# Performance work log

Hardware: AMD Instinct MI355X
Metric: run time of the kernel (lower is better)

Reference implementation:

```python
import jax, jax.numpy as jnp
import numpy as np

L, H, NH, HD, FF, S, B, V, NL = 2, 2048, 16, 128, 4096, 1024, 2, 32000, 4
R, SCALING, BLK = 2, 16.0 / 2.0, 64  # LoRA r=2, alpha=16 -> scaling 8; NF4 blocksize 64
NF4 = jnp.array([-1.0, -0.6961928009986877, -0.5250730514526367, -0.39491748809814453,
                 -0.28444138169288635, -0.18477343022823334, -0.09105003625154495, 0.0,
                 0.07958029955625534, 0.16093020141124725, 0.24611230194568634,
                 0.33791524171829224, 0.44070982933044434, 0.5626170039176941,
                 0.7229568362236023, 1.0], dtype=jnp.float32)

def dequant(codes, scales):
    # codes [out, in] int -> NF4 values; scales [out, in//BLK] absmax per 64-block
    return NF4[codes] * jnp.repeat(scales, BLK, axis=-1)

def qlin(x, codes, scales, A, Bm):
    # fused dequant + GEMM + LoRA low-rank update: x @ (Wd + s*B@A).T
    W = dequant(codes, scales)
    return x @ W.T + SCALING * ((x @ A.T) @ Bm.T)

def layer_norm(x, g, b):
    mu = jnp.mean(x, -1, keepdims=True)
    var = jnp.var(x, -1, keepdims=True)
    return (x - mu) * jax.lax.rsqrt(var + 1e-5) * g + b

def rope(x):  # x [B,S,NH,HD]
    half = HD // 2
    inv = 1.0 / (10000.0 ** (jnp.arange(half, dtype=jnp.float32) / half))
    ang = jnp.arange(S, dtype=jnp.float32)[:, None] * inv[None, :]
    cos = jnp.concatenate([jnp.cos(ang)] * 2, -1)[None, :, None, :]
    sin = jnp.concatenate([jnp.sin(ang)] * 2, -1)[None, :, None, :]
    x1, x2 = x[..., :half], x[..., half:]
    return x * cos + jnp.concatenate([-x2, x1], -1) * sin

def setup_inputs() -> dict:
    key = jax.random.key(0)
    it = iter(jax.random.split(key, 64))
    nrm = lambda shp, s: jax.random.normal(next(it), shp, jnp.float32) * s
    cod = lambda shp: jax.random.randint(next(it), shp, 0, 16, jnp.int32)
    scl = lambda shp: jax.random.uniform(next(it), shp, jnp.float32) * 0.02 + 1e-3
    lens = jax.random.randint(next(it), (B,), S // 2, S + 1)
    return dict(
        input_ids=jax.random.randint(next(it), (B, S), 0, V, jnp.int32),
        attention_mask=(jnp.arange(S)[None, :] < lens[:, None]).astype(jnp.int32),
        labels=jax.random.randint(next(it), (B,), 0, NL, jnp.int32),
        embed=nrm((V, H), 0.02),
        qkv_codes=cod((L, 3 * H, H)), qkv_scales=scl((L, 3 * H, H // BLK)),
        qkv_A=nrm((L, R, H), 0.01), qkv_B=nrm((L, 3 * H, R), 0.01),
        dense_codes=cod((L, H, H)), dense_scales=scl((L, H, H // BLK)),
        dense_A=nrm((L, R, H), 0.01), dense_B=nrm((L, H, R), 0.01),
        min_codes=cod((L, 2 * FF, H)), min_scales=scl((L, 2 * FF, H // BLK)),
        min_A=nrm((L, R, H), 0.01), min_B=nrm((L, 2 * FF, R), 0.01),
        mout_codes=cod((L, H, FF)), mout_scales=scl((L, H, FF // BLK)),
        mout_A=nrm((L, R, FF), 0.01), mout_B=nrm((L, H, R), 0.01),
        ln1_g=jnp.ones((L, H)), ln1_b=jnp.zeros((L, H)),
        ln2_g=jnp.ones((L, H)), ln2_b=jnp.zeros((L, H)),
        lnf_g=jnp.ones((H,)), lnf_b=jnp.zeros((H,)),
        classifier_w=nrm((NL, H), 0.01),
    )

def reference(input_ids, attention_mask, labels, embed, qkv_codes, qkv_scales, qkv_A, qkv_B,
              dense_codes, dense_scales, dense_A, dense_B, min_codes, min_scales, min_A, min_B,
              mout_codes, mout_scales, mout_A, mout_B, ln1_g, ln1_b, ln2_g, ln2_b,
              lnf_g, lnf_b, classifier_w):
    x = embed[input_ids]  # [B,S,H]
    mask = jnp.tril(jnp.ones((S, S), bool))[None, None] & (attention_mask[:, None, None, :] > 0)
    for l in range(L):
        h = layer_norm(x, ln1_g[l], ln1_b[l])
        qkv = qlin(h, qkv_codes[l], qkv_scales[l], qkv_A[l], qkv_B[l]).reshape(B, S, NH, 3 * HD)
        q, k, v = qkv[..., :HD], qkv[..., HD:2 * HD], qkv[..., 2 * HD:]
        q, k = rope(q), rope(k)
        scores = jnp.einsum('bqhd,bkhd->bhqk', q, k) / np.float32(np.sqrt(HD))
        probs = jax.nn.softmax(jnp.where(mask, scores, jnp.float32(-1e30)), -1)
        attn = jnp.einsum('bhqk,bkhd->bqhd', probs, v).reshape(B, S, H)
        x = x + qlin(attn, dense_codes[l], dense_scales[l], dense_A[l], dense_B[l])
        h2 = layer_norm(x, ln2_g[l], ln2_b[l])
        u = qlin(h2, min_codes[l], min_scales[l], min_A[l], min_B[l])  # [B,S,2*FF] packed SwiGLU
        g = jax.nn.silu(u[..., :FF]) * u[..., FF:]
        x = x + qlin(g, mout_codes[l], mout_scales[l], mout_A[l], mout_B[l])
    x = layer_norm(x, lnf_g, lnf_b)
    eos = x[jnp.arange(B), attention_mask.sum(1) - 1]  # last non-padded token hidden
    logits = eos @ classifier_w.T
    logp = jax.nn.log_softmax(logits, -1)
    loss = -jnp.mean(logp[jnp.arange(B), labels])
    return loss, logits
```

## Files before the change

kernel.cpp:

```cpp
#include <hip/hip_runtime.h>

typedef unsigned short u16;
typedef __attribute__((ext_vector_type(4))) float f32x4;
typedef __attribute__((ext_vector_type(8))) short short8;
typedef __attribute__((ext_vector_type(4))) short short4v;

constexpr int CL  = 2;
constexpr int CH  = 2048;
constexpr int CNH = 16;
constexpr int CHD = 128;
constexpr int CFF = 4096;
constexpr int CS  = 1024;
constexpr int CB  = 2;
constexpr int CNL = 4;
constexpr int CM  = CB * CS;
#define SCALING 8.0f

__device__ __constant__ float NF4TAB[16] = {
    -1.0f, -0.6961928009986877f, -0.5250730514526367f, -0.39491748809814453f,
    -0.28444138169288635f, -0.18477343022823334f, -0.09105003625154495f, 0.0f,
    0.07958029955625534f, 0.16093020141124725f, 0.24611230194568634f,
    0.33791524171829224f, 0.44070982933044434f, 0.5626170039176941f,
    0.7229568362236023f, 1.0f};

__device__ __forceinline__ u16 f2bf(float f) {
  union { float f; unsigned u; } v; v.f = f;
  unsigned r = v.u + 0x7fffu + ((v.u >> 16) & 1u);
  return (u16)(r >> 16);
}
__device__ __forceinline__ float bf2f(u16 u) {
  union { unsigned u; float f; } v; v.u = ((unsigned)u) << 16;
  return v.f;
}

template <int N> __device__ __forceinline__ void wait_vm() {
  if constexpr (N == 0)      asm volatile("s_waitcnt vmcnt(0)" ::: "memory");
  else if constexpr (N == 6) asm volatile("s_waitcnt vmcnt(6)" ::: "memory");
  else if constexpr (N == 8) asm volatile("s_waitcnt vmcnt(8)" ::: "memory");
  else                       asm volatile("s_waitcnt vmcnt(0)" ::: "memory");
}

__device__ __forceinline__ float blockReduceSum(float v) {
  __shared__ float sh[4];
  #pragma unroll
  for (int o = 32; o > 0; o >>= 1) v += __shfl_down(v, o);
  __syncthreads();
  if ((threadIdx.x & 63) == 0) sh[threadIdx.x >> 6] = v;
  __syncthreads();
  return sh[0] + sh[1] + sh[2] + sh[3];
}

__global__ void k_embed(const int* __restrict__ ids, const float* __restrict__ emb,
                        float* __restrict__ x) {
  int m = blockIdx.x;
  const float4* src = (const float4*)(emb + (size_t)ids[m] * CH);
  float4* dst = (float4*)(x + (size_t)m * CH);
  for (int i = threadIdx.x; i < CH / 4; i += 256) dst[i] = src[i];
}

__global__ void k_ln_xa(const float* __restrict__ x, const float* __restrict__ g,
                        const float* __restrict__ b, const float* __restrict__ A,
                        u16* __restrict__ o, float* __restrict__ xA) {
  int m = blockIdx.x, tid = threadIdx.x;
  const float* row = x + (size_t)m * CH;
  float s = 0.f, s2 = 0.f;
  for (int i = tid; i < CH / 4; i += 256) {
    float4 v = ((const float4*)row)[i];
    s += v.x + v.y + v.z + v.w;
    s2 += v.x * v.x + v.y * v.y + v.z * v.z + v.w * v.w;
  }
  s = blockReduceSum(s);
  s2 = blockReduceSum(s2);
  float mu = s / CH, var = s2 / CH - mu * mu;
  float rs = rsqrtf(var + 1e-5f);
  u16* orow = o + (size_t)m * CH;
  float s0 = 0.f, s1 = 0.f;
  for (int i = tid; i < CH / 4; i += 256) {
    float4 v = ((const float4*)row)[i];
    float4 gv = ((const float4*)g)[i];
    float4 bv = ((const float4*)b)[i];
    float4 a0 = ((const float4*)A)[i];
    float4 a1 = ((const float4*)(A + CH))[i];
    float h0 = (v.x - mu) * rs * gv.x + bv.x;
    float h1 = (v.y - mu) * rs * gv.y + bv.y;
    float h2 = (v.z - mu) * rs * gv.z + bv.z;
    float h3 = (v.w - mu) * rs * gv.w + bv.w;
    short4v ov = { (short)f2bf(h0), (short)f2bf(h1), (short)f2bf(h2), (short)f2bf(h3) };
    *(short4v*)(orow + i * 4) = ov;
    s0 += h0 * a0.x + h1 * a0.y + h2 * a0.z + h3 * a0.w;
    s1 += h0 * a1.x + h1 * a1.y + h2 * a1.z + h3 * a1.w;
  }
  s0 = blockReduceSum(s0);
  s1 = blockReduceSum(s1);
  if (tid == 0) { xA[2 * m] = s0; xA[2 * m + 1] = s1; }
}

__global__ void k_xa(const u16* __restrict__ xb, const float* __restrict__ A,
                     float* __restrict__ xA, int K) {
  int m = blockIdx.x, tid = threadIdx.x;
  const u16* row = xb + (size_t)m * K;
  float s0 = 0.f, s1 = 0.f;
  for (int c = tid; c < K / 8; c += 256) {
    short8 v = *(const short8*)(row + c * 8);
    #pragma unroll
    for (int e = 0; e < 8; ++e) {
      float f = bf2f((u16)v[e]);
      s0 += f * A[c * 8 + e];
      s1 += f * A[K + c * 8 + e];
    }
  }
  s0 = blockReduceSum(s0);
  s1 = blockReduceSum(s1);
  if (tid == 0) { xA[2 * m] = s0; xA[2 * m + 1] = s1; }
}

__global__ void k_dequant(const int* __restrict__ codes, const float* __restrict__ scales,
                          u16* __restrict__ w, int kshift, long total) {
  __shared__ float lut[16];
  if (threadIdx.x < 16) lut[threadIdx.x] = NF4TAB[threadIdx.x];
  __syncthreads();
  long base = ((long)blockIdx.x * 256 + threadIdx.x) * 8;
  if (base >= total) return;
  long n = base >> kshift;
  int k = (int)(base & ((1L << kshift) - 1));
  float sc = scales[(size_t)n * (1 << (kshift - 6)) + (k >> 6)];
  const int* cp = codes + base;
  short8 o;
  #pragma unroll
  for (int i = 0; i < 8; ++i) o[i] = (short)f2bf(lut[cp[i] & 15] * sc);
  *(short8*)(w + base) = o;
}

__global__ void k_ropetab(float* __restrict__ cosT, float* __restrict__ sinT) {
  int i = blockIdx.x * 256 + threadIdx.x;
  if (i >= CS * 64) return;
  int s = i >> 6, d = i & 63;
  float inv = powf(10000.0f, -(float)d / 64.0f);
  float a = (float)s * inv;
  cosT[i] = cosf(a);
  sinT[i] = sinf(a);
}

__global__ void k_rope(const u16* __restrict__ qkv, const float* __restrict__ cosT,
                       const float* __restrict__ sinT, u16* __restrict__ Qb,
                       u16* __restrict__ Kb) {
  int bid = blockIdx.x;
  int s = bid & (CS - 1);
  int z = bid >> 10;
  int b = z >> 4, h = z & 15;
  int d = threadIdx.x;
  const u16* base = qkv + ((size_t)(b * CS + s)) * (3 * CH) + h * (3 * CHD);
  int dh = d & 63;
  float c = cosT[s * 64 + dh], sn = sinT[s * 64 + dh];
  float sgn = (d < 64) ? -1.0f : 1.0f;
  float q = bf2f(base[d]),       qp = bf2f(base[d ^ 64]);
  float k = bf2f(base[CHD + d]), kp = bf2f(base[CHD + (d ^ 64)]);
  size_t oi = ((size_t)z * CS + s) * CHD + d;
  Qb[oi] = f2bf(q * c + sgn * qp * sn);
  Kb[oi] = f2bf(k * c + sgn * kp * sn);
}

__global__ void k_vtrans(const u16* __restrict__ qkv, u16* __restrict__ Vt) {
  __shared__ u16 tile[32][33];
  int z = blockIdx.z;
  int b = z >> 4, h = z & 15;
  int s0 = blockIdx.x * 32, d0 = blockIdx.y * 32;
  int tx = threadIdx.x, ty = threadIdx.y;
  #pragma unroll
  for (int i = 0; i < 32; i += 8)
    tile[ty + i][tx] =
        qkv[((size_t)(b * CS + s0 + ty + i)) * (3 * CH) + h * (3 * CHD) + 2 * CHD + d0 + tx];
  __syncthreads();
  #pragma unroll
  for (int i = 0; i < 32; i += 8)
    Vt[((size_t)z * CHD + d0 + ty + i) * CS + s0 + tx] = tile[tx][ty + i];
}

__global__ __launch_bounds__(256, 2) void k_flash(
    const u16* __restrict__ Qb, const u16* __restrict__ Kb, const u16* __restrict__ Vt,
    const int* __restrict__ amask, u16* __restrict__ out) {
  __shared__ u16 Ks[64 * 128];
  __shared__ u16 Vs[128 * 64];
  __shared__ float bias[CS];
  __shared__ u16 Ps[4][16][80];
  int bid = blockIdx.x;
  int qt = 15 - (bid >> 5);
  int z = bid & 31;
  int b = z >> 4, h = z & 15;
  int tid = threadIdx.x, lane = tid & 63, wid = tid >> 6;
  int lrow = lane & 15, lgrp = lane >> 4;
  const u16* Qz = Qb + (size_t)z * CS * CHD;
  const u16* Kz = Kb + (size_t)z * CS * CHD;
  const u16* Vz = Vt + (size_t)z * CHD * CS;

  for (int i = tid; i < CS; i += 256)
    bias[i] = amask[b * CS + i] ? 0.f : -1e30f;

  int qrow = qt * 64 + wid * 16 + lrow;
  short8 qf[4];
  #pragma unroll
  for (int kk = 0; kk < 4; ++kk)
    qf[kk] = *(const short8*)(Qz + (size_t)qrow * CHD + kk * 32 + lgrp * 8);

  float m_r[4], l_r[4];
  #pragma unroll
  for (int r = 0; r < 4; ++r) { m_r[r] = -3e38f; l_r[r] = 0.f; }
  f32x4 o_acc[8];
  #pragma unroll
  for (int dj = 0; dj < 8; ++dj) o_acc[dj] = (f32x4){0.f, 0.f, 0.f, 0.f};

  const float SCL = 0.08838834764831845f;

  short8 kA[4], vA[4];
  #pragma unroll
  for (int it = 0; it < 4; ++it) {
    int c = it * 256 + tid;
    kA[it] = *(const short8*)(Kz + (size_t)(c >> 4) * CHD + (c & 15) * 8);
    vA[it] = *(const short8*)(Vz + (size_t)(c >> 3) * CS + (c & 7) * 8);
  }

  for (int t = 0; t <= qt; ++t) {
    int k0 = t * 64;
    __syncthreads();
    #pragma unroll
    for (int it = 0; it < 4; ++it) {
      int c = it * 256 + tid;
      int key = c >> 4, ch = c & 15;
      *(short8*)((char*)Ks + key * 256 + ((ch * 16) ^ ((key & 7) << 4))) = kA[it];
      int d = c >> 3, ch2 = c & 7;
      *(short8*)((char*)Vs + d * 128 + ((ch2 * 16) ^ ((d & 7) << 4))) = vA[it];
    }
    short8 kB[4], vB[4];
    if (t < qt) {
      int k1 = k0 + 64;
      #pragma unroll
      for (int it = 0; it < 4; ++it) {
        int c = it * 256 + tid;
        kB[it] = *(const short8*)(Kz + (size_t)(k1 + (c >> 4)) * CHD + (c & 15) * 8);
        vB[it] = *(const short8*)(Vz + (size_t)(c >> 3) * CS + k1 + (c & 7) * 8);
      }
    }
    __syncthreads();

    f32x4 s_acc[4];
    #pragma unroll
    for (int nj = 0; nj < 4; ++nj) s_acc[nj] = (f32x4){0.f, 0.f, 0.f, 0.f};
    #pragma unroll
    for (int kk = 0; kk < 4; ++kk) {
      #pragma unroll
      for (int nj = 0; nj < 4; ++nj) {
        int key = nj * 16 + lrow;
        short8 kf = *(const short8*)((const char*)Ks + key * 256 +
                                     (((kk * 32 + lgrp * 8) * 2) ^ ((key & 7) << 4)));
        s_acc[nj] = __builtin_amdgcn_mfma_f32_16x16x32_bf16(qf[kk], kf, s_acc[nj], 0, 0, 0);
      }
    }

    bool diag = (t == qt);
    float p[4][4], mx[4];
    #pragma unroll
    for (int r = 0; r < 4; ++r) {
      int ql = wid * 16 + 4 * lgrp + r;
      float rm = -3e38f;
      #pragma unroll
      for (int nj = 0; nj < 4; ++nj) {
        int kl = nj * 16 + lrow;
        float v = s_acc[nj][r] * SCL + bias[k0 + kl];
        if (diag && kl > ql) v = -1e30f;
        p[nj][r] = v;
        rm = fmaxf(rm, v);
      }
      mx[r] = rm;
    }
    #pragma unroll
    for (int o = 1; o < 16; o <<= 1)
      #pragma unroll
      for (int r = 0; r < 4; ++r) mx[r] = fmaxf(mx[r], __shfl_xor(mx[r], o));
    float ps[4], alpha[4];
    #pragma unroll
    for (int r = 0; r < 4; ++r) {
      float mn = fmaxf(m_r[r], mx[r]);
      alpha[r] = __expf(m_r[r] - mn);
      m_r[r] = mn;
      float acc = 0.f;
      #pragma unroll
      for (int nj = 0; nj < 4; ++nj) {
        float e = __expf(p[nj][r] - mn);
        p[nj][r] = e;
        acc += e;
      }
      ps[r] = acc;
    }
    #pragma unroll
    for (int o = 1; o < 16; o <<= 1)
      #pragma unroll
      for (int r = 0; r < 4; ++r) ps[r] += __shfl_xor(ps[r], o);
    #pragma unroll
    for (int r = 0; r < 4; ++r) {
      l_r[r] = l_r[r] * alpha[r] + ps[r];
      #pragma unroll
      for (int dj = 0; dj < 8; ++dj) o_acc[dj][r] *= alpha[r];
    }

    #pragma unroll
    for (int r = 0; r < 4; ++r)
      #pragma unroll
      for (int nj = 0; nj < 4; ++nj)
        Ps[wid][4 * lgrp + r][nj * 16 + lrow] = f2bf(p[nj][r]);
    #pragma unroll
    for (int kk2 = 0; kk2 < 2; ++kk2) {
      short8 pa = *(const short8*)(&Ps[wid][lrow][kk2 * 32 + lgrp * 8]);
      #pragma unroll
      for (int dj = 0; dj < 8; ++dj) {
        int d = dj * 16 + lrow;
        short8 vf = *(const short8*)((const char*)Vs + d * 128 +
                                     (((kk2 * 32 + lgrp * 8) * 2) ^ ((d & 7) << 4)));
        o_acc[dj] = __builtin_amdgcn_mfma_f32_16x16x32_bf16(pa, vf, o_acc[dj], 0, 0, 0);
      }
    }

    if (t < qt) {
      #pragma unroll
      for (int it = 0; it < 4; ++it) { kA[it] = kB[it]; vA[it] = vB[it]; }
    }
  }

  #pragma unroll
  for (int r = 0; r < 4; ++r) {
    float inv = 1.0f / l_r[r];
    int qg = qt * 64 + wid * 16 + 4 * lgrp + r;
    size_t rowoff = ((size_t)(b * CS + qg)) * CH + h * CHD;
    #pragma unroll
    for (int dj = 0; dj < 8; ++dj)
      out[rowoff + dj * 16 + lrow] = f2bf(o_acc[dj][r] * inv);
  }
}

__global__ void k_silu_xa(const u16* __restrict__ u, const float* __restrict__ A,
                          u16* __restrict__ g, float* __restrict__ xA) {
  int m = blockIdx.x, tid = threadIdx.x;
  const u16* urow = u + (size_t)m * (2 * CFF);
  u16* grow = g + (size_t)m * CFF;
  float s0 = 0.f, s1 = 0.f;
  for (int c = tid; c < CFF / 8; c += 256) {
    short8 va = *(const short8*)(urow + c * 8);
    short8 vb = *(const short8*)(urow + CFF + c * 8);
    short8 og;
    #pragma unroll
    for (int e = 0; e < 8; ++e) {
      float a = bf2f((u16)va[e]);
      float bb = bf2f((u16)vb[e]);
      float gg = (a / (1.0f + __expf(-a))) * bb;
      og[e] = (short)f2bf(gg);
      s0 += gg * A[c * 8 + e];
      s1 += gg * A[CFF + c * 8 + e];
    }
    *(short8*)(grow + c * 8) = og;
  }
  s0 = blockReduceSum(s0);
  s1 = blockReduceSum(s1);
  if (tid == 0) { xA[2 * m] = s0; xA[2 * m + 1] = s1; }
}

template <int BM, int BN, int TW, int WM, int WN, int OUT_BF16, int LORA, int RESID>
__global__ __launch_bounds__(TW, 2) void k_gemm3(
    const u16* __restrict__ Ag, const u16* __restrict__ Bg, void* __restrict__ Cout,
    const float* __restrict__ resid, const float* __restrict__ xA,
    const float* __restrict__ lB, int K, int N) {
  constexpr int WROWS = BM / WM, WCOLS = BN / WN;
  constexpr int M_REP = WROWS / 16, N_REP = WCOLS / 16;
  constexpr int LA = BM * 8 / TW, LBN = BN * 8 / TW;
  constexpr int LPT = LA + LBN;
  __shared__ __align__(16) u16 As[2][BM * 64];
  __shared__ __align__(16) u16 Bs[2][BN * 64];
  int tid = threadIdx.x, lane = tid & 63, wid = tid >> 6;
  int wm = wid / WN, wn = wid % WN;
  int gx = gridDim.x, nwg = gx * gridDim.y;
  int bid = blockIdx.y * gx + blockIdx.x;
  int qq = nwg >> 3, rr = nwg & 7;
  int xcd = bid & 7, lid = bid >> 3;
  int swz = (xcd < rr ? xcd * (qq + 1) : rr * (qq + 1) + (xcd - rr) * qq) + lid;
  long bm = (long)(swz % gx) * BM, bn = (long)(swz / gx) * BN;

  f32x4 acc[M_REP][N_REP];
  #pragma unroll
  for (int i = 0; i < M_REP; ++i)
    #pragma unroll
    for (int j = 0; j < N_REP; ++j) acc[i][j] = (f32x4){0.f, 0.f, 0.f, 0.f};

  auto stage = [&](int buf, int t) {
    int k0 = t * 64;
    #pragma unroll
    for (int i = 0; i < LA; ++i) {
      int f = i * TW + tid;
      int r = f >> 3, g = (f & 7) ^ (r & 7);
      __builtin_amdgcn_global_load_lds(
          (const __attribute__((address_space(1))) void*)(Ag + (size_t)(bm + r) * K + k0 + g * 8),
          (__attribute__((address_space(3))) void*)(&As[buf][f * 8]), 16, 0, 0);
    }
    #pragma unroll
    for (int i = 0; i < LBN; ++i) {
      int f = i * TW + tid;
      int r = f >> 3, g = (f & 7) ^ (r & 7);
      __builtin_amdgcn_global_load_lds(
          (const __attribute__((address_space(1))) void*)(Bg + (size_t)(bn + r) * K + k0 + g * 8),
          (__attribute__((address_space(3))) void*)(&Bs[buf][f * 8]), 16, 0, 0);
    }
  };

  int NT = K >> 6;
  stage(0, 0);
  stage(1, 1);

  int kg = lane >> 4, lr = lane & 15;
  for (int t = 0; t < NT; ++t) {
    int buf = t & 1;
    if (t + 1 < NT) wait_vm<LPT>();
    else            wait_vm<0>();
    __builtin_amdgcn_s_barrier();

    short8 af[2][M_REP], bfr[2][N_REP];
    #pragma unroll
    for (int kk = 0; kk < 2; ++kk) {
      int au = kk * 4 + kg;
      #pragma unroll
      for (int i = 0; i < M_REP; ++i) {
        int r = wm * WROWS + i * 16 + lr;
        af[kk][i] = *(const short8*)(&As[buf][r * 64 + ((au ^ (r & 7)) << 3)]);
      }
      #pragma unroll
      for (int j = 0; j < N_REP; ++j) {
        int r = wn * WCOLS + j * 16 + lr;
        bfr[kk][j] = *(const short8*)(&Bs[buf][r * 64 + ((au ^ (r & 7)) << 3)]);
      }
    }
    asm volatile("s_waitcnt lgkmcnt(0)" ::: "memory");
    __builtin_amdgcn_s_barrier();
    if (t + 2 < NT) stage(buf, t + 2);

    __builtin_amdgcn_s_setprio(1);
    #pragma unroll
    for (int kk = 0; kk < 2; ++kk)
      #pragma unroll
      for (int i = 0; i < M_REP; ++i)
        #pragma unroll
        for (int j = 0; j < N_REP; ++j)
          acc[i][j] = __builtin_amdgcn_mfma_f32_16x16x32_bf16(af[kk][i], bfr[kk][j], acc[i][j], 0, 0, 0);
    __builtin_amdgcn_s_setprio(0);
  }

  #pragma unroll
  for (int i = 0; i < M_REP; ++i) {
    #pragma unroll
    for (int r = 0; r < 4; ++r) {
      long m = bm + wm * WROWS + i * 16 + ((lane >> 4) << 2) + r;
      float xa0 = 0.f, xa1 = 0.f;
      if (LORA) { xa0 = xA[2 * m]; xa1 = xA[2 * m + 1]; }
      #pragma unroll
      for (int j = 0; j < N_REP; ++j) {
        long n = bn + wn * WCOLS + j * 16 + (lane & 15);
        float v = acc[i][j][r];
        if (LORA) v += SCALING * (xa0 * lB[2 * n] + xa1 * lB[2 * n + 1]);
        if (RESID) v += resid[m * N + n];
        if (OUT_BF16)
          ((u16*)Cout)[m * N + n] = f2bf(v);
        else
          ((float*)Cout)[m * N + n] = v;
      }
    }
  }
}

#define RD_A(d, mh)                                                              \
  { _Pragma("unroll") for (int kk = 0; kk < 2; ++kk) {                           \
      _Pragma("unroll") for (int ii = 0; ii < 4; ++ii) {                         \
        int ra = ((mh) * 4 + ii) * 16 + lr;                                      \
        int slot = (kk * 4 + kg) ^ (ra & 7);                                     \
        a_f[kk][ii] = *(const short8*)(&As[d][wm][ra * 64 + slot * 8]);          \
      } } }
#define RD_B(d, nh)                                                              \
  { _Pragma("unroll") for (int kk = 0; kk < 2; ++kk) {                           \
      _Pragma("unroll") for (int jj = 0; jj < 2; ++jj) {                         \
        int rb = (wn & 1) * 64 + ((nh) * 2 + jj) * 16 + lr;                      \
        int slot = (kk * 4 + kg) ^ (rb & 7);                                     \
        b_f[nh][kk][jj] = *(const short8*)(&Bs[d][wn >> 1][rb * 64 + slot * 8]); \
      } } }
#define MFMA_Q(mh, nh)                                                           \
  { __builtin_amdgcn_s_setprio(1);                                               \
    _Pragma("unroll") for (int kk = 0; kk < 2; ++kk) {                           \
      _Pragma("unroll") for (int ii = 0; ii < 4; ++ii) {                         \
        _Pragma("unroll") for (int jj = 0; jj < 2; ++jj) {                       \
          acc[(mh) * 4 + ii][(nh) * 2 + jj] =                                    \
              __builtin_amdgcn_mfma_f32_16x16x32_bf16(                           \
                  a_f[kk][ii], b_f[nh][kk][jj],                                  \
                  acc[(mh) * 4 + ii][(nh) * 2 + jj], 0, 0, 0);                   \
        } } }                                                                    \
    __builtin_amdgcn_s_setprio(0); }
#define LGKM0_SB                                                                 \
  asm volatile("s_waitcnt lgkmcnt(0)" ::: "memory");                             \
  __builtin_amdgcn_sched_barrier(0);
#define BAR __builtin_amdgcn_s_barrier();

__global__ __launch_bounds__(512, 2) void k_gemm8(
    const u16* __restrict__ Ag, const u16* __restrict__ Bg, u16* __restrict__ Cout,
    const float* __restrict__ xA, const float* __restrict__ lB, int K, int N) {
  __shared__ __align__(16) u16 As[2][2][128 * 64];
  __shared__ __align__(16) u16 Bs[2][2][128 * 64];
  int tid = threadIdx.x, lane = tid & 63, wid = tid >> 6;
  int wm = wid >> 2, wn = wid & 3;
  int kg = lane >> 4, lr = lane & 15;
  int gx = gridDim.x, nwg = gx * gridDim.y;
  int bid = blockIdx.y * gx + blockIdx.x;
  int qq = nwg >> 3, rr = nwg & 7;
  int xcd = bid & 7, lid = bid >> 3;
  int swz = (xcd < rr ? xcd * (qq + 1) : rr * (qq + 1) + (xcd - rr) * qq) + lid;
  long bm = (long)(swz % gx) * 256, bn = (long)(swz / gx) * 256;
  const int NKT = K >> 6;

  f32x4 acc[8][4];
  #pragma unroll
  for (int i = 0; i < 8; ++i)
    #pragma unroll
    for (int j = 0; j < 4; ++j) acc[i][j] = (f32x4){0.f, 0.f, 0.f, 0.f};
  short8 a_f[2][4], b_f[2][2][2];

  auto stA = [&](int t, int h) {
    int d = t & 1;
    int tt = t < NKT ? t : NKT - 1;
    int k0 = tt << 6;
    #pragma unroll
    for (int ld = 0; ld < 2; ++ld) {
      int f = ld * 512 + tid;
      int row = f >> 3, p = f & 7;
      int ss = p ^ (row & 7);
      __builtin_amdgcn_global_load_lds(
          (const __attribute__((address_space(1))) void*)(Ag + (size_t)(bm + h * 128 + row) * K + k0 + ss * 8),
          (__attribute__((address_space(3))) void*)(&As[d][h][f * 8]), 16, 0, 0);
    }
  };
  auto stB = [&](int t, int h) {
    int d = t & 1;
    int tt = t < NKT ? t : NKT - 1;
    int k0 = tt << 6;
    #pragma unroll
    for (int ld = 0; ld < 2; ++ld) {
      int f = ld * 512 + tid;
      int row = f >> 3, p = f & 7;
      int ss = p ^ (row & 7);
      __builtin_amdgcn_global_load_lds(
          (const __attribute__((address_space(1))) void*)(Bg + (size_t)(bn + h * 128 + row) * K + k0 + ss * 8),
          (__attribute__((address_space(3))) void*)(&Bs[d][h][f * 8]), 16, 0, 0);
    }
  };

  stA(0, 0); stA(0, 1); stB(0, 0); stB(0, 1);
  stB(1, 0); stA(1, 0);
  asm volatile("s_waitcnt vmcnt(4)" ::: "memory");
  BAR

  int NI = NKT >> 1;
  for (int j = 0; j < NI; ++j) {
    int t0 = 2 * j;
    RD_A(0, 0) RD_B(0, 0)
    stA(t0 + 1, 1);
    BAR LGKM0_SB MFMA_Q(0, 0) BAR
    RD_B(0, 1)
    stB(t0 + 1, 1);
    BAR LGKM0_SB MFMA_Q(0, 1) BAR
    RD_A(0, 1)
    stB(t0 + 2, 0);
    BAR LGKM0_SB MFMA_Q(1, 0) BAR
    stA(t0 + 2, 0);
    asm volatile("s_waitcnt vmcnt(4)" ::: "memory");
    BAR MFMA_Q(1, 1) BAR
    RD_A(1, 0) RD_B(1, 0)
    stA(t0 + 2, 1);
    BAR LGKM0_SB MFMA_Q(0, 0) BAR
    RD_B(1, 1)
    stB(t0 + 2, 1);
    BAR LGKM0_SB MFMA_Q(0, 1) BAR
    RD_A(1, 1)
    stB(t0 + 3, 0);
    BAR LGKM0_SB MFMA_Q(1, 0) BAR
    stA(t0 + 3, 0);
    asm volatile("s_waitcnt vmcnt(4)" ::: "memory");
    BAR MFMA_Q(1, 1) BAR
  }

  #pragma unroll
  for (int i = 0; i < 8; ++i) {
    #pragma unroll
    for (int r = 0; r < 4; ++r) {
      long m = bm + wm * 128 + i * 16 + ((lane >> 4) << 2) + r;
      float xa0 = xA[2 * m], xa1 = xA[2 * m + 1];
      #pragma unroll
      for (int j = 0; j < 4; ++j) {
        long n = bn + wn * 64 + j * 16 + (lane & 15);
        float v = acc[i][j][r] + SCALING * (xa0 * lB[2 * n] + xa1 * lB[2 * n + 1]);
        Cout[m * N + n] = f2bf(v);
      }
    }
  }
}

__global__ void k_final(const float* __restrict__ x, const int* __restrict__ amask,
                        const int* __restrict__ labels, const float* __restrict__ g,
                        const float* __restrict__ bb, const float* __restrict__ cw,
                        float* __restrict__ out) {
  __shared__ float xr[CH];
  __shared__ float lg[CB][CNL];
  int tid = threadIdx.x;
  for (int b = 0; b < CB; ++b) {
    float fc = 0.f;
    for (int k = tid; k < CS; k += 256) fc += (amask[b * CS + k] != 0) ? 1.0f : 0.0f;
    int len = (int)(blockReduceSum(fc) + 0.5f);
    const float* row = x + ((size_t)b * CS + (len - 1)) * CH;
    float s = 0.f, s2 = 0.f;
    for (int k = tid; k < CH; k += 256) { float v = row[k]; s += v; s2 += v * v; }
    s = blockReduceSum(s);
    s2 = blockReduceSum(s2);
    float mu = s / CH, var = s2 / CH - mu * mu;
    float rs = rsqrtf(var + 1e-5f);
    for (int k = tid; k < CH; k += 256) xr[k] = (row[k] - mu) * rs * g[k] + bb[k];
    __syncthreads();
    for (int c = 0; c < CNL; ++c) {
      float p = 0.f;
      for (int k = tid; k < CH; k += 256) p += xr[k] * cw[c * CH + k];
      p = blockReduceSum(p);
      if (tid == 0) { lg[b][c] = p; out[1 + b * CNL + c] = p; }
    }
    __syncthreads();
  }
  if (tid == 0) {
    float loss = 0.f;
    for (int b = 0; b < CB; ++b) {
      float mx = -1e30f;
      for (int c = 0; c < CNL; ++c) mx = fmaxf(mx, lg[b][c]);
      float se = 0.f;
      for (int c = 0; c < CNL; ++c) se += expf(lg[b][c] - mx);
      float lse = mx + logf(se);
      loss -= (lg[b][labels[b]] - lse);
    }
    out[0] = loss / CB;
  }
}

static constexpr size_t X_OFF  = 0;
static constexpr size_t H_OFF  = X_OFF + (size_t)CM * CH * 4;
static constexpr size_t W_OFF  = H_OFF + (size_t)CM * CH * 2;
static constexpr size_t SC_OFF = W_OFF + (size_t)8192 * 2048 * 2;
static constexpr size_t PR_OFF = SC_OFF + (size_t)32 * CS * CS * 4;
static constexpr size_t XA_OFF = PR_OFF + (size_t)32 * CS * CS * 2;
static constexpr size_t CS_OFF = XA_OFF + (size_t)CM * 2 * 4;
static constexpr size_t SN_OFF = CS_OFF + (size_t)CS * 64 * 4;
static constexpr size_t WS_END = SN_OFF + (size_t)CS * 64 * 4;

extern "C" void kernel_launch(void* const* d_in, const int* in_sizes, int n_in,
                              void* d_out, int out_size, void* d_ws, size_t ws_size,
                              hipStream_t stream) {
  (void)in_sizes; (void)n_in; (void)out_size;
  if (ws_size < WS_END) return;

  const int*   ids          = (const int*)d_in[0];
  const int*   amask        = (const int*)d_in[1];
  const int*   labels       = (const int*)d_in[2];
  const float* emb          = (const float*)d_in[3];
  const int*   qkv_codes    = (const int*)d_in[4];
  const float* qkv_scales   = (const float*)d_in[5];
  const float* qkv_A        = (const float*)d_in[6];
  const float* qkv_B        = (const float*)d_in[7];
  const int*   dense_codes  = (const int*)d_in[8];
  const float* dense_scales = (const float*)d_in[9];
  const float* dense_A      = (const float*)d_in[10];
  const float* dense_B      = (const float*)d_in[11];
  const int*   min_codes    = (const int*)d_in[12];
  const float* min_scales   = (const float*)d_in[13];
  const float* min_A        = (const float*)d_in[14];
  const float* min_B        = (const float*)d_in[15];
  const int*   mout_codes   = (const int*)d_in[16];
  const float* mout_scales  = (const float*)d_in[17];
  const float* mout_A       = (const float*)d_in[18];
  const float* mout_B       = (const float*)d_in[19];
  const float* ln1_g        = (const float*)d_in[20];
  const float* ln1_b        = (const float*)d_in[21];
  const float* ln2_g        = (const float*)d_in[22];
  const float* ln2_b        = (const float*)d_in[23];
  const float* lnf_g        = (const float*)d_in[24];
  const float* lnf_b        = (const float*)d_in[25];
  const float* cw           = (const float*)d_in[26];

  char* ws = (char*)d_ws;
  float* x       = (float*)(ws + X_OFF);
  u16*   hbuf    = (u16*)(ws + H_OFF);
  u16*   wbuf    = (u16*)(ws + W_OFF);
  u16*   Qb      = (u16*)(ws + W_OFF);
  u16*   Kb      = (u16*)(ws + W_OFF + (size_t)32 * CS * CHD * 2);
  u16*   Vt      = (u16*)(ws + W_OFF + (size_t)64 * CS * CHD * 2);
  u16*   qkv_out = (u16*)(ws + SC_OFF);
  u16*   ubuf    = (u16*)(ws + SC_OFF);
  u16*   gbuf    = (u16*)(ws + PR_OFF);
  float* xA      = (float*)(ws + XA_OFF);
  float* cosT    = (float*)(ws + CS_OFF);
  float* sinT    = (float*)(ws + SN_OFF);

  k_ropetab<<<(CS * 64 + 255) / 256, 256, 0, stream>>>(cosT, sinT);
  k_embed<<<CM, 256, 0, stream>>>(ids, emb, x);

  for (int l = 0; l < CL; ++l) {
    k_ln_xa<<<CM, 256, 0, stream>>>(x, ln1_g + l * CH, ln1_b + l * CH,
                                    qkv_A + (size_t)l * 2 * CH, hbuf, xA);
    long nq = (long)3 * CH * CH;
    k_dequant<<<(int)(nq / 8 / 256), 256, 0, stream>>>(
        qkv_codes + (size_t)l * nq, qkv_scales + (size_t)l * 3 * CH * (CH / 64),
        wbuf, 11, nq);
    k_gemm3<128, 128, 256, 2, 2, 1, 1, 0><<<dim3(CM / 128, (3 * CH) / 128), 256, 0, stream>>>(
        hbuf, wbuf, qkv_out, nullptr, xA, qkv_B + (size_t)l * 3 * CH * 2, CH, 3 * CH);
    k_rope<<<32 * CS, 128, 0, stream>>>(qkv_out, cosT, sinT, Qb, Kb);
    k_vtrans<<<dim3(CS / 32, CHD / 32, 32), dim3(32, 8), 0, stream>>>(qkv_out, Vt);
    k_flash<<<512, 256, 0, stream>>>(Qb, Kb, Vt, amask, hbuf);
    k_xa<<<CM, 256, 0, stream>>>(hbuf, dense_A + (size_t)l * 2 * CH, xA, CH);
    long nd = (long)CH * CH;
    k_dequant<<<(int)(nd / 8 / 256), 256, 0, stream>>>(
        dense_codes + (size_t)l * nd, dense_scales + (size_t)l * CH * (CH / 64),
        wbuf, 11, nd);
    k_gemm3<128, 64, 256, 2, 2, 0, 1, 1><<<dim3(CM / 128, CH / 64), 256, 0, stream>>>(
        hbuf, wbuf, x, x, xA, dense_B + (size_t)l * CH * 2, CH, CH);

    k_ln_xa<<<CM, 256, 0, stream>>>(x, ln2_g + l * CH, ln2_b + l * CH,
                                    min_A + (size_t)l * 2 * CH, hbuf, xA);
    long nm = (long)2 * CFF * CH;
    k_dequant<<<(int)(nm / 8 / 256), 256, 0, stream>>>(
        min_codes + (size_t)l * nm, min_scales + (size_t)l * 2 * CFF * (CH / 64),
        wbuf, 11, nm);
    k_gemm8<<<dim3(CM / 256, (2 * CFF) / 256), 512, 0, stream>>>(
        hbuf, wbuf, ubuf, xA, min_B + (size_t)l * 2 * CFF * 2, CH, 2 * CFF);
    k_silu_xa<<<CM, 256, 0, stream>>>(ubuf, mout_A + (size_t)l * 2 * CFF, gbuf, xA);
    long no = (long)CH * CFF;
    k_dequant<<<(int)(no / 8 / 256), 256, 0, stream>>>(
        mout_codes + (size_t)l * no, mout_scales + (size_t)l * CH * (CFF / 64),
        wbuf, 12, no);
    k_gemm3<128, 64, 256, 2, 2, 0, 1, 1><<<dim3(CM / 128, CH / 64), 256, 0, stream>>>(
        gbuf, wbuf, x, x, xA, mout_B + (size_t)l * CH * 2, CFF, CH);
  }

  k_final<<<1, 256, 0, stream>>>(x, amask, labels, lnf_g, lnf_b, cw, (float*)d_out);
}
```

Baseline: 750.9 us.

## Split flash attention along the key dimension and combine partials in a second kernel

The attention kernel now splits each query tile's key range into up to four chunks of four key tiles. Each chunk runs as its own block and writes unnormalized fp32 output plus the per-row max and sum. A new combine kernel rescales and merges the partials into the bf16 output. This spreads the causal load more evenly across more blocks, at the cost of extra global traffic for the fp32 partials and one more launch. The post-load __syncthreads is also replaced by an explicit lgkmcnt wait plus s_barrier with sched_barriers.

```diff
diff --git a/kernel.cpp b/kernel.cpp
--- a/kernel.cpp
+++ b/kernel.cpp
@@ -176,25 +176,31 @@
     Vt[((size_t)z * CHD + d0 + ty + i) * CS + s0 + tx] = tile[tx][ty + i];
 }
 
-__global__ __launch_bounds__(256, 2) void k_flash(
+__global__ __launch_bounds__(256, 2) void k_flashp(
     const u16* __restrict__ Qb, const u16* __restrict__ Kb, const u16* __restrict__ Vt,
-    const int* __restrict__ amask, u16* __restrict__ out) {
+    const int* __restrict__ amask, float* __restrict__ Opart, float* __restrict__ mlpart) {
+  int bid = blockIdx.x;
+  int sp = bid & 3;
+  int z  = (bid >> 2) & 31;
+  int qt = bid >> 7;
+  int t0 = sp * 4;
+  if (t0 > qt) return;
+  int t1 = min(qt + 1, t0 + 4);
+  int b = z >> 4, h = z & 15;
   __shared__ u16 Ks[64 * 128];
   __shared__ u16 Vs[128 * 64];
-  __shared__ float bias[CS];
+  __shared__ float bias[256];
   __shared__ u16 Ps[4][16][80];
-  int bid = blockIdx.x;
-  int qt = 15 - (bid >> 5);
-  int z = bid & 31;
-  int b = z >> 4, h = z & 15;
   int tid = threadIdx.x, lane = tid & 63, wid = tid >> 6;
   int lrow = lane & 15, lgrp = lane >> 4;
   const u16* Qz = Qb + (size_t)z * CS * CHD;
   const u16* Kz = Kb + (size_t)z * CS * CHD;
   const u16* Vz = Vt + (size_t)z * CHD * CS;
 
-  for (int i = tid; i < CS; i += 256)
-    bias[i] = amask[b * CS + i] ? 0.f : -1e30f;
+  {
+    int k = t0 * 64 + tid;
+    bias[tid] = amask[b * CS + k] ? 0.f : -1e30f;
+  }
 
   int qrow = qt * 64 + wid * 16 + lrow;
   short8 qf[4];
@@ -215,11 +221,11 @@
   #pragma unroll
   for (int it = 0; it < 4; ++it) {
     int c = it * 256 + tid;
-    kA[it] = *(const short8*)(Kz + (size_t)(c >> 4) * CHD + (c & 15) * 8);
-    vA[it] = *(const short8*)(Vz + (size_t)(c >> 3) * CS + (c & 7) * 8);
-  }
-
-  for (int t = 0; t <= qt; ++t) {
+    kA[it] = *(const short8*)(Kz + (size_t)(t0 * 64 + (c >> 4)) * CHD + (c & 15) * 8);
+    vA[it] = *(const short8*)(Vz + (size_t)(c >> 3) * CS + t0 * 64 + (c & 7) * 8);
+  }
+
+  for (int t = t0; t < t1; ++t) {
     int k0 = t * 64;
     __syncthreads();
     #pragma unroll
@@ -231,7 +237,7 @@
       *(short8*)((char*)Vs + d * 128 + ((ch2 * 16) ^ ((d & 7) << 4))) = vA[it];
     }
     short8 kB[4], vB[4];
-    if (t < qt) {
+    if (t + 1 < t1) {
       int k1 = k0 + 64;
       #pragma unroll
       for (int it = 0; it < 4; ++it) {
@@ -240,7 +246,10 @@
         vB[it] = *(const short8*)(Vz + (size_t)(c >> 3) * CS + k1 + (c & 7) * 8);
       }
     }
-    __syncthreads();
+    asm volatile("s_waitcnt lgkmcnt(0)" ::: "memory");
+    __builtin_amdgcn_sched_barrier(0);
+    __builtin_amdgcn_s_barrier();
+    __builtin_amdgcn_sched_barrier(0);
 
     f32x4 s_acc[4];
     #pragma unroll
@@ -265,7 +274,7 @@
       #pragma unroll
       for (int nj = 0; nj < 4; ++nj) {
         int kl = nj * 16 + lrow;
-        float v = s_acc[nj][r] * SCL + bias[k0 + kl];
+        float v = s_acc[nj][r] * SCL + bias[(k0 - t0 * 64) + kl];
         if (diag && kl > ql) v = -1e30f;
         p[nj][r] = v;
         rm = fmaxf(rm, v);
@@ -319,20 +328,47 @@
       }
     }
 
-    if (t < qt) {
+    if (t + 1 < t1) {
       #pragma unroll
       for (int it = 0; it < 4; ++it) { kA[it] = kB[it]; vA[it] = vB[it]; }
     }
   }
 
+  int part = (z * 16 + qt) * 4 + sp;
+  float* Op = Opart + (size_t)part * 64 * 128;
+  float* ml = mlpart + (size_t)part * 128;
   #pragma unroll
   for (int r = 0; r < 4; ++r) {
-    float inv = 1.0f / l_r[r];
-    int qg = qt * 64 + wid * 16 + 4 * lgrp + r;
-    size_t rowoff = ((size_t)(b * CS + qg)) * CH + h * CHD;
+    int row = wid * 16 + 4 * lgrp + r;
     #pragma unroll
     for (int dj = 0; dj < 8; ++dj)
-      out[rowoff + dj * 16 + lrow] = f2bf(o_acc[dj][r] * inv);
+      Op[row * 128 + dj * 16 + lrow] = o_acc[dj][r];
+    if (lrow == 0) { ml[row * 2] = m_r[r]; ml[row * 2 + 1] = l_r[r]; }
+  }
+}
+
+__global__ void k_fcomb(const float* __restrict__ Opart, const float* __restrict__ mlpart,
+                        u16* __restrict__ out) {
+  int zq = blockIdx.x;
+  int z = zq >> 4, qt = zq & 15;
+  int b = z >> 4, h = z & 15;
+  int ns = (qt >> 2) + 1;
+  int tid = threadIdx.x;
+  int c = tid & 127, r0 = tid >> 7;
+  for (int r = r0; r < 64; r += 2) {
+    float M = -3e38f;
+    for (int s = 0; s < ns; ++s)
+      M = fmaxf(M, mlpart[(size_t)((z * 16 + qt) * 4 + s) * 128 + r * 2]);
+    float L = 0.f, O = 0.f;
+    for (int s = 0; s < ns; ++s) {
+      int part = (z * 16 + qt) * 4 + s;
+      float mm = mlpart[(size_t)part * 128 + r * 2];
+      float ll = mlpart[(size_t)part * 128 + r * 2 + 1];
+      float w = __expf(mm - M);
+      L += ll * w;
+      O += Opart[(size_t)part * 64 * 128 + r * 128 + c] * w;
+    }
+    out[((size_t)(b * CS + qt * 64 + r)) * CH + h * CHD + c] = f2bf(O / L);
   }
 }
 
@@ -698,7 +734,9 @@
   u16*   Vt      = (u16*)(ws + W_OFF + (size_t)64 * CS * CHD * 2);
   u16*   qkv_out = (u16*)(ws + SC_OFF);
   u16*   ubuf    = (u16*)(ws + SC_OFF);
+  float* Opart   = (float*)(ws + SC_OFF);
   u16*   gbuf    = (u16*)(ws + PR_OFF);
+  float* mlpart  = (float*)(ws + PR_OFF);
   float* xA      = (float*)(ws + XA_OFF);
   float* cosT    = (float*)(ws + CS_OFF);
   float* sinT    = (float*)(ws + SN_OFF);
@@ -717,7 +755,8 @@
         hbuf, wbuf, qkv_out, nullptr, xA, qkv_B + (size_t)l * 3 * CH * 2, CH, 3 * CH);
     k_rope<<<32 * CS, 128, 0, stream>>>(qkv_out, cosT, sinT, Qb, Kb);
     k_vtrans<<<dim3(CS / 32, CHD / 32, 32), dim3(32, 8), 0, stream>>>(qkv_out, Vt);
-    k_flash<<<512, 256, 0, stream>>>(Qb, Kb, Vt, amask, hbuf);
+    k_flashp<<<2048, 256, 0, stream>>>(Qb, Kb, Vt, amask, Opart, mlpart);
+    k_fcomb<<<512, 256, 0, stream>>>(Opart, mlpart, hbuf);
     k_xa<<<CM, 256, 0, stream>>>(hbuf, dense_A + (size_t)l * 2 * CH, xA, CH);
     long nd = (long)CH * CH;
     k_dequant<<<(int)(nd / 8 / 256), 256, 0, stream>>>(
```

Measured after the change: 932.5 us. 24.2% more time.
